# Performance work log

Measured on AMD Instinct MI355X. Metric: run time of the kernel, lower is better.

The kernel has to match this reference:

```python
import math
import jax, jax.numpy as jnp
import numpy as np


def setup_inputs() -> dict:
    key = jax.random.key(0)
    k1, k2, k3, k4 = jax.random.split(key, 4)
    B, C, H, W = 8, 256, 128, 128
    norm_dim, K = 64, 3
    return {
        "fea": jax.random.normal(k1, (B, C, H, W), dtype=jnp.float32),
        "norm_feat": jax.random.normal(k2, (B, norm_dim, 1, 1), dtype=jnp.float32),
        "mod_w": jax.random.normal(k3, (C, norm_dim, 1, 1), dtype=jnp.float32),
        "mod_b": jnp.zeros((C,), dtype=jnp.float32),
        "weight": jax.random.normal(k4, (1, C, C, K, K), dtype=jnp.float32),
    }


def reference(fea, norm_feat, mod_w, mod_b, weight):
    B, C, H, W = fea.shape
    K = weight.shape[-1]
    scale = 1.0 / math.sqrt(C * K * K)
    # 1x1 modulation conv on (B, norm_dim, 1, 1) -> style (B, C)
    style = jnp.einsum('bdhw,cd->bc', norm_feat, mod_w[:, :, 0, 0]) + mod_b  # (B, C)
    # modulate: (1, C_out, C_in, K, K) * (B, 1, C_in, 1, 1)
    w = scale * weight * style[:, None, :, None, None]  # (B, C, C, K, K)
    demod = jax.lax.rsqrt(jnp.sum(w * w, axis=(2, 3, 4)) + 1e-8)  # (B, C)
    w = w * demod[:, :, None, None, None]
    # grouped-conv trick: groups=B, input (1, B*C, H, W), weight (B*C, C, K, K)
    w = w.reshape(B * C, C, K, K)
    x = fea.reshape(1, B * C, H, W)
    out = jax.lax.conv_general_dilated(
        x, w,
        window_strides=(1, 1),
        padding=[(K // 2, K // 2), (K // 2, K // 2)],
        dimension_numbers=('NCHW', 'OIHW', 'NCHW'),
        feature_group_count=B,
    )
    return out.reshape(B, C, H, W)
```

## Files before the change

### kernel.cpp

```cpp
#include <hip/hip_runtime.h>

typedef unsigned short u16;
typedef unsigned int u32;
typedef short s8v __attribute__((ext_vector_type(8)));
typedef float f16v __attribute__((ext_vector_type(16)));
typedef u32 u32x4 __attribute__((ext_vector_type(4)));

__device__ __forceinline__ u16 f2bf(float f) {
    u32 u = __float_as_uint(f);
    u += 0x7FFFu + ((u >> 16) & 1u);
    return (u16)(u >> 16);
}

__device__ __forceinline__ void async_load16(const u16* g, u16* l) {
    __builtin_amdgcn_global_load_lds(
        (const __attribute__((address_space(1))) u32*)g,
        (__attribute__((address_space(3))) u32*)l,
        16, 0, 0);
}

__global__ void style_kernel(const float* __restrict__ norm_feat,
                             const float* __restrict__ mod_w,
                             const float* __restrict__ mod_b,
                             float* __restrict__ style) {
    __shared__ float nf[64];
    __shared__ float mw[256][65];
    const int b = blockIdx.x;
    const int tid = threadIdx.x;

    if (tid < 64) nf[tid] = norm_feat[b * 64 + tid];
    #pragma unroll
    for (int i = 0; i < 64; ++i) {
        int idx = i * 256 + tid;
        mw[idx >> 6][idx & 63] = mod_w[idx];
    }
    __syncthreads();

    float s = mod_b[tid];
    #pragma unroll 8
    for (int d = 0; d < 64; ++d) s += nf[d] * mw[tid][d];
    style[b * 256 + tid] = s;
}

__global__ void modulate_kernel(const float* __restrict__ style,
                                const float* __restrict__ weight,
                                u16* __restrict__ Wmod) {
    const int co = blockIdx.x;
    const int b  = blockIdx.y;
    const int ci = threadIdx.x;

    __shared__ float red[256];

    const float s = style[b * 256 + ci];

    float w9[9];
    const float* wp = weight + ((size_t)co * 256 + ci) * 9;
    float sq = 0.f;
    #pragma unroll
    for (int t = 0; t < 9; ++t) { w9[t] = wp[t]; sq += w9[t] * w9[t]; }

    red[ci] = sq * s * s;
    __syncthreads();
    for (int off = 128; off > 0; off >>= 1) {
        if (ci < off) red[ci] += red[ci + off];
        __syncthreads();
    }
    const float scale = 1.0f / 48.0f;
    const float demod = rsqrtf(scale * scale * red[0] + 1e-8f);
    const float coef  = scale * s * demod;

    const size_t tile = (((size_t)b * 9 * 8 + (co >> 5)) * 16 + (ci >> 4)) * 512
                      + (size_t)((co & 31) + 32 * ((ci >> 3) & 1)) * 8 + (ci & 7);
    #pragma unroll
    for (int t = 0; t < 9; ++t) {
        Wmod[tile + (size_t)t * 65536] = f2bf(w9[t] * coef);
    }
}

__global__ __launch_bounds__(256) void transpose_kernel(const float* __restrict__ fea,
                                                        u16* __restrict__ feaT) {
    __shared__ float lds_t[64][132];
    const int y = blockIdx.x;
    const int b = blockIdx.y;
    const int tid = threadIdx.x;

    for (int c0 = 0; c0 < 256; c0 += 64) {
        #pragma unroll
        for (int r = 0; r < 8; ++r) {
            int i  = r * 256 + tid;
            int c  = i >> 5;
            int x4 = i & 31;
            float4 v = *(const float4*)&fea[(((size_t)(b * 256 + c0 + c)) * 128 + y) * 128 + x4 * 4];
            *(float4*)&lds_t[c][x4 * 4] = v;
        }
        __syncthreads();
        #pragma unroll
        for (int jj = 0; jj < 4; ++jj) {
            int p   = jj * 256 + tid;
            int x   = p & 127;
            int g   = p >> 7;
            int cb8 = g * 8;
            u32x4 wv;
            #pragma unroll
            for (int k = 0; k < 4; ++k) {
                float f0 = lds_t[cb8 + 2 * k][x];
                float f1 = lds_t[cb8 + 2 * k + 1][x];
                wv[k] = (u32)f2bf(f0) | ((u32)f2bf(f1) << 16);
            }
            int c  = c0 + cb8;
            int ch = c >> 4;
            int cg = (c >> 3) & 1;
            size_t off = (((((size_t)b * 128 + y) * 16 + ch) * 2 + cg) * 128 + x) * 8;
            *(u32x4*)&feaT[off] = wv;
        }
        __syncthreads();
    }
}

__global__ __launch_bounds__(512, 4) void conv_mfma(
        const u16* __restrict__ Wmod,
        const u16* __restrict__ feaT,
        float* __restrict__ out) {
    __shared__ u16 lds[2][4][2][128][8];
    __shared__ u16 zpad[8];

    const int lin = blockIdx.x + 64 * (blockIdx.y + 2 * blockIdx.z);
    const int nid = (lin & 7) * 128 + (lin >> 3);
    const int yp  = nid & 63;
    const int cbk = (nid >> 6) & 1;
    const int b   = nid >> 7;

    const int tid  = threadIdx.x;
    const int lane = tid & 63;
    const int wave = tid >> 6;
    const int mw  = wave & 1;
    const int nw  = (wave >> 1) & 1;
    const int yw  = wave >> 2;
    const int l31 = lane & 31;
    const int l5  = lane >> 5;

    if (tid < 8) zpad[tid] = 0;

    const int y_out = 2 * yp + yw;
    const bool rokv[3] = { (y_out > 0), true, (y_out < 127) };

    const u16* Abase = Wmod + (size_t)b * 9 * 65536
                            + (size_t)(cbk * 4 + mw * 2) * 8192 + (size_t)lane * 8;

    auto loadA = [&](int t, int i, int ch) -> s8v {
        return *(const s8v*)(Abase + (size_t)t * 65536 + (size_t)i * 8192 + (size_t)ch * 512);
    };

    auto stage = [&](int buf, int ch) {
        u16* ldsb = &lds[buf][0][0][0][0];
        #pragma unroll
        for (int i = 0; i < 2; ++i) {
            int u  = wave + 8 * i;
            int r  = u >> 2;
            int cg = (u >> 1) & 1;
            int xq = u & 1;
            int gy = 2 * yp - 1 + r;
            if ((unsigned)gy < 128u) {
                const u16* g = feaT +
                    (((((size_t)b * 128 + gy) * 16 + ch) * 2 + cg) * 128 + xq * 64) * 8
                    + (size_t)lane * 8;
                async_load16(g, ldsb + ((r * 2 + cg) * 128 + xq * 64) * 8);
            }
        }
    };

    f16v acc[2][2];
    #pragma unroll
    for (int i = 0; i < 2; ++i)
        #pragma unroll
        for (int j = 0; j < 2; ++j) acc[i][j] = (f16v)0.0f;

    s8v fr[3][2];

    stage(0, 0);
    #pragma unroll
    for (int g = 0; g < 3; ++g) {
        fr[g][0] = loadA(g, 0, 0);
        fr[g][1] = loadA(g, 1, 0);
    }
    __syncthreads();

    const int xb0 = nw * 64 + l31 - 1;

    #pragma unroll 1
    for (int ch = 0; ch < 16; ++ch) {
        const u16* bufp = &lds[ch & 1][0][0][0][0];
        #pragma unroll
        for (int t = 0; t < 9; ++t) {
            const int kh = t / 3, kw = t % 3;
            const int rr = kh + yw;
            const bool rok = rokv[kh];

            s8v bfr[2];
            #pragma unroll
            for (int j = 0; j < 2; ++j) {
                int x_in = xb0 + j * 32 + kw;
                bool v = rok && ((unsigned)x_in < 128u);
                const u16* bp = v ? (bufp + (((rr * 2 + l5) * 128 + x_in) * 8)) : zpad;
                bfr[j] = *(const s8v*)bp;
            }

            #pragma unroll
            for (int i = 0; i < 2; ++i)
                #pragma unroll
                for (int j = 0; j < 2; ++j)
                    acc[i][j] = __builtin_amdgcn_mfma_f32_32x32x16_bf16(
                        fr[t % 3][i], bfr[j], acc[i][j], 0, 0, 0);

            if (t < 6) {
                fr[t % 3][0] = loadA(t + 3, 0, ch);
                fr[t % 3][1] = loadA(t + 3, 1, ch);
            } else if (ch < 15) {
                fr[t % 3][0] = loadA(t - 6, 0, ch + 1);
                fr[t % 3][1] = loadA(t - 6, 1, ch + 1);
            }

            if (t == 3 && ch < 15) stage((ch + 1) & 1, ch + 1);
        }
        __syncthreads();
    }

    const int x_base = nw * 64 + l31;
    #pragma unroll
    for (int i = 0; i < 2; ++i) {
        #pragma unroll
        for (int j = 0; j < 2; ++j) {
            #pragma unroll
            for (int reg = 0; reg < 16; ++reg) {
                int co = cbk * 128 + mw * 64 + i * 32 + (reg & 3) + 8 * (reg >> 2) + 4 * l5;
                out[(((size_t)(b * 256 + co) * 128 + y_out) * 128) + x_base + j * 32] = acc[i][j][reg];
            }
        }
    }
}

extern "C" void kernel_launch(void* const* d_in, const int* in_sizes, int n_in,
                              void* d_out, int out_size, void* d_ws, size_t ws_size,
                              hipStream_t stream) {
    const float* fea       = (const float*)d_in[0];
    const float* norm_feat = (const float*)d_in[1];
    const float* mod_w     = (const float*)d_in[2];
    const float* mod_b     = (const float*)d_in[3];
    const float* weight    = (const float*)d_in[4];
    float* out = (float*)d_out;

    u16* Wmod = (u16*)d_ws;
    u16* feaT = (u16*)((char*)d_ws + 9u * 1024u * 1024u);
    float* style = (float*)feaT;

    style_kernel<<<dim3(8), 256, 0, stream>>>(norm_feat, mod_w, mod_b, style);
    modulate_kernel<<<dim3(256, 8), 256, 0, stream>>>(style, weight, Wmod);
    transpose_kernel<<<dim3(128, 8), 256, 0, stream>>>(fea, feaT);
    conv_mfma<<<dim3(64, 2, 8), 512, 0, stream>>>(Wmod, feaT, out);
}
```

Measured before the change: 386.2 us.

## Precompute LDS B-fragment offsets, raise MFMA priority, relax end-of-chunk barrier wait

Replaces the per-tap bounds checks and separate zero-pad buffer with offsets precomputed per kernel row, pointing out-of-range reads at a zero region appended to each LDS buffer. MFMA groups are wrapped in s_setprio so the wave gets issue priority during matrix work. The full __syncthreads at the end of each channel chunk becomes a partial vmcnt wait plus s_barrier, so A-fragment prefetches for the next chunk can stay in flight. The partial vmcnt count must still cover the async global-to-LDS loads, or later reads could see stale data.

```diff
diff --git a/kernel.cpp b/kernel.cpp
--- a/kernel.cpp
+++ b/kernel.cpp
@@ -121,8 +121,7 @@
         const u16* __restrict__ Wmod,
         const u16* __restrict__ feaT,
         float* __restrict__ out) {
-    __shared__ u16 lds[2][4][2][128][8];
-    __shared__ u16 zpad[8];
+    __shared__ u16 lds[2][8216];
 
     const int lin = blockIdx.x + 64 * (blockIdx.y + 2 * blockIdx.z);
     const int nid = (lin & 7) * 128 + (lin >> 3);
@@ -139,10 +138,24 @@
     const int l31 = lane & 31;
     const int l5  = lane >> 5;
 
-    if (tid < 8) zpad[tid] = 0;
+    if (tid < 24) { lds[0][8192 + tid] = 0; lds[1][8192 + tid] = 0; }
 
     const int y_out = 2 * yp + yw;
-    const bool rokv[3] = { (y_out > 0), true, (y_out < 127) };
+
+    const int xb0 = nw * 64 + l31 - 1;
+    int ofj0[3], ofj1[3], bq0[3], bq2[3];
+    #pragma unroll
+    for (int kh = 0; kh < 3; ++kh) {
+        const int rr = kh + yw;
+        const int rowb = ((rr * 2 + l5) * 128) * 8;
+        const bool rok = (kh == 0) ? (y_out > 0) : (kh == 2 ? (y_out < 127) : true);
+        const int o0 = rowb + xb0 * 8;
+        const int o1 = o0 + 256;
+        ofj0[kh] = rok ? o0 : 8192;
+        ofj1[kh] = rok ? o1 : 8192;
+        bq0[kh]  = (rok && xb0 >= 0)       ? o0        : 8192;
+        bq2[kh]  = (rok && xb0 + 34 < 128) ? (o1 + 16) : 8192;
+    }
 
     const u16* Abase = Wmod + (size_t)b * 9 * 65536
                             + (size_t)(cbk * 4 + mw * 2) * 8192 + (size_t)lane * 8;
@@ -152,7 +165,7 @@
     };
 
     auto stage = [&](int buf, int ch) {
-        u16* ldsb = &lds[buf][0][0][0][0];
+        u16* ldsb = &lds[buf][0];
         #pragma unroll
         for (int i = 0; i < 2; ++i) {
             int u  = wave + 8 * i;
@@ -185,32 +198,29 @@
     }
     __syncthreads();
 
-    const int xb0 = nw * 64 + l31 - 1;
-
     #pragma unroll 1
     for (int ch = 0; ch < 16; ++ch) {
-        const u16* bufp = &lds[ch & 1][0][0][0][0];
+        const u16* basep = &lds[ch & 1][0];
         #pragma unroll
         for (int t = 0; t < 9; ++t) {
             const int kh = t / 3, kw = t % 3;
-            const int rr = kh + yw;
-            const bool rok = rokv[kh];
 
             s8v bfr[2];
-            #pragma unroll
-            for (int j = 0; j < 2; ++j) {
-                int x_in = xb0 + j * 32 + kw;
-                bool v = rok && ((unsigned)x_in < 128u);
-                const u16* bp = v ? (bufp + (((rr * 2 + l5) * 128 + x_in) * 8)) : zpad;
-                bfr[j] = *(const s8v*)bp;
-            }
-
+            {
+                const u16* a0 = (kw == 0) ? (basep + bq0[kh]) : (basep + ofj0[kh] + kw * 8);
+                const u16* a1 = (kw == 2) ? (basep + bq2[kh]) : (basep + ofj1[kh] + kw * 8);
+                bfr[0] = *(const s8v*)a0;
+                bfr[1] = *(const s8v*)a1;
+            }
+
+            __builtin_amdgcn_s_setprio(1);
             #pragma unroll
             for (int i = 0; i < 2; ++i)
                 #pragma unroll
                 for (int j = 0; j < 2; ++j)
                     acc[i][j] = __builtin_amdgcn_mfma_f32_32x32x16_bf16(
                         fr[t % 3][i], bfr[j], acc[i][j], 0, 0, 0);
+            __builtin_amdgcn_s_setprio(0);
 
             if (t < 6) {
                 fr[t % 3][0] = loadA(t + 3, 0, ch);
@@ -220,9 +230,19 @@
                 fr[t % 3][1] = loadA(t - 6, 1, ch + 1);
             }
 
-            if (t == 3 && ch < 15) stage((ch + 1) & 1, ch + 1);
-        }
-        __syncthreads();
+            if (t == 3 && ch < 15) {
+                __builtin_amdgcn_sched_barrier(0);
+                stage((ch + 1) & 1, ch + 1);
+                __builtin_amdgcn_sched_barrier(0);
+            }
+        }
+
+        if (ch < 15) {
+            asm volatile("s_waitcnt vmcnt(6)" ::: "memory");
+            __builtin_amdgcn_sched_barrier(0);
+            __builtin_amdgcn_s_barrier();
+            __builtin_amdgcn_sched_barrier(0);
+        }
     }
 
     const int x_base = nw * 64 + l31;
```

New measurement: 378.9 us. Within noise of the previous version (-1.9%).
